# Performance work log

Measured on AMD Instinct MI355X. Metric: run time of the kernel, lower is better.

## Reference

```python
import jax, jax.numpy as jnp
import numpy as np
from jax import lax

B = 2; CIN = 1; IMG = 96; P = 8; EMB = 384; NH = 8; HD = EMB // NH
NL = 6; MLP = 4 * EMB; NC = 2
NPATCH = (IMG // P) ** 3  # 1728
N = NPATCH + 1            # 1729 tokens (cls + patches)


def setup_inputs() -> dict:
    key = jax.random.key(0)
    ks = iter(jax.random.split(key, 16))
    def nrm(shape, scale=0.02):
        return jax.random.normal(next(ks), shape, jnp.float32) * scale
    inp = {}
    inp["x"] = jax.random.normal(next(ks), (B, CIN, IMG, IMG, IMG), jnp.float32)
    inp["conv_w"] = nrm((EMB, CIN, P, P, P))
    inp["conv_b"] = jnp.zeros((EMB,), jnp.float32)
    inp["cls_token"] = nrm((1, 1, EMB))
    inp["pos_embed"] = nrm((1, N, EMB))
    inp["ln1_w"] = jnp.ones((NL, EMB), jnp.float32)
    inp["ln1_b"] = jnp.zeros((NL, EMB), jnp.float32)
    inp["qkv_w"] = nrm((NL, 3 * EMB, EMB))
    inp["qkv_b"] = jnp.zeros((NL, 3 * EMB), jnp.float32)
    inp["proj_w"] = nrm((NL, EMB, EMB))
    inp["proj_b"] = jnp.zeros((NL, EMB), jnp.float32)
    inp["ln2_w"] = jnp.ones((NL, EMB), jnp.float32)
    inp["ln2_b"] = jnp.zeros((NL, EMB), jnp.float32)
    inp["mlp_w1"] = nrm((NL, MLP, EMB))
    inp["mlp_b1"] = jnp.zeros((NL, MLP), jnp.float32)
    inp["mlp_w2"] = nrm((NL, EMB, MLP))
    inp["mlp_b2"] = jnp.zeros((NL, EMB), jnp.float32)
    inp["norm_w"] = jnp.ones((EMB,), jnp.float32)
    inp["norm_b"] = jnp.zeros((EMB,), jnp.float32)
    inp["head_w"] = nrm((NC, EMB))
    inp["head_b"] = jnp.zeros((NC,), jnp.float32)
    return inp


def _ln(x, w, b, eps=1e-5):
    mu = jnp.mean(x, axis=-1, keepdims=True)
    var = jnp.mean((x - mu) ** 2, axis=-1, keepdims=True)
    return (x - mu) * lax.rsqrt(var + eps) * w + b


def reference(x, conv_w, conv_b, cls_token, pos_embed,
              ln1_w, ln1_b, qkv_w, qkv_b, proj_w, proj_b,
              ln2_w, ln2_b, mlp_w1, mlp_b1, mlp_w2, mlp_b2,
              norm_w, norm_b, head_w, head_b):
    b = x.shape[0]
    # Conv3d patch embedding (kernel == stride)
    xp = lax.conv_general_dilated(
        x, conv_w, window_strides=(P, P, P), padding='VALID',
        dimension_numbers=('NCDHW', 'OIDHW', 'NCDHW'))
    xp = xp + conv_b[None, :, None, None, None]
    t = xp.reshape(b, EMB, NPATCH).transpose(0, 2, 1)  # [B, NPATCH, EMB]
    cls = jnp.broadcast_to(cls_token, (b, 1, EMB))
    t = jnp.concatenate([cls, t], axis=1) + pos_embed   # [B, N, EMB]
    scale = HD ** -0.5
    for i in range(NL):
        # --- attention block ---
        h = _ln(t, ln1_w[i], ln1_b[i])
        qkv = (h @ qkv_w[i].T + qkv_b[i]).reshape(b, N, 3, NH, HD)
        q, k, v = qkv[:, :, 0], qkv[:, :, 1], qkv[:, :, 2]  # [B, N, NH, HD]
        scores = jnp.einsum('bnhd,bmhd->bhnm', q, k) * scale
        attn = jax.nn.softmax(scores, axis=-1)
        o = jnp.einsum('bhnm,bmhd->bnhd', attn, v).reshape(b, N, EMB)
        t = t + (o @ proj_w[i].T + proj_b[i])
        # --- MLP block ---
        h = _ln(t, ln2_w[i], ln2_b[i])
        h = jax.nn.gelu(h @ mlp_w1[i].T + mlp_b1[i], approximate=False)
        t = t + (h @ mlp_w2[i].T + mlp_b2[i])
    t = _ln(t, norm_w, norm_b)
    logits = t[:, 0] @ head_w.T + head_b  # [B, NC]
    return logits
```

## Files before the change

kernel.cpp:

```cpp
#include <hip/hip_runtime.h>
#include <math.h>

#define B_      2
#define EMB_    384
#define NH_     8
#define HD_     48
#define NTOK    1729
#define NPATCH_ 1728
#define MLP_    1536
#define NL_     6
#define NC_     2
#define BSTR    1792
#define M_PAD   3584
#define SCALE_  0.14433756729740643f
#define OPSZ    ((size_t)B_ * BSTR * EMB_)

typedef __bf16 bf16x8 __attribute__((ext_vector_type(8)));
typedef float floatx4 __attribute__((ext_vector_type(4)));
typedef _Float16 halfx4 __attribute__((ext_vector_type(4)));
typedef unsigned short u16;

__device__ __forceinline__ u16 f2b(float f) {
    unsigned int u = __float_as_uint(f);
    return (u16)((u + 0x7FFFu + ((u >> 16) & 1u)) >> 16);
}
__device__ __forceinline__ u16 f2h(float f) {
    _Float16 h = (_Float16)f;
    return __builtin_bit_cast(unsigned short, h);
}
__device__ __forceinline__ bf16x8 ld8(const u16* p) {
    return *(const bf16x8*)p;
}

#define CW_N  196608
#define P0_   196608
#define P1_   1966080
#define P2_   4620288
#define P3_   5505024
#define P4_   9043968
#define P5_   12582912
__global__ __launch_bounds__(256) void cvt_all(
    const float* __restrict__ cw, const float* __restrict__ x,
    const float* __restrict__ qw, const float* __restrict__ pw,
    const float* __restrict__ w1, const float* __restrict__ w2,
    u16* __restrict__ cwb, u16* __restrict__ xb, u16* __restrict__ qwb,
    u16* __restrict__ pwb, u16* __restrict__ w1b, u16* __restrict__ w2b)
{
    int i = (blockIdx.x * 256 + threadIdx.x) * 4;
    const float* s; u16* d; int off;
    if      (i < P0_) { s = cw; d = cwb; off = 0; }
    else if (i < P1_) { s = x;  d = xb;  off = P0_; }
    else if (i < P2_) { s = qw; d = qwb; off = P1_; }
    else if (i < P3_) { s = pw; d = pwb; off = P2_; }
    else if (i < P4_) { s = w1; d = w1b; off = P3_; }
    else              { s = w2; d = w2b; off = P4_; }
    i -= off;
    float4 v = *(const float4*)(s + i);
    ushort4 o;
    o.x = f2b(v.x); o.y = f2b(v.y); o.z = f2b(v.z); o.w = f2b(v.w);
    *(ushort4*)(d + i) = o;
}

__global__ __launch_bounds__(256) void patch_mfma(
    const u16* __restrict__ xb, const u16* __restrict__ cwb,
    const float* __restrict__ cb, const float* __restrict__ cls,
    const float* __restrict__ pos, float* __restrict__ t)
{
    __shared__ __align__(16) u16 As[64][40];
    __shared__ __align__(16) u16 Bs[64][40];
    const int tid  = threadIdx.x;
    const int lane = tid & 63, w = tid >> 6;
    const int wm = (w >> 1) * 32, wn = (w & 1) * 32;
    const int m0g = blockIdx.y * 64, n0g = blockIdx.x * 64;
    const int cl = lane & 15, kh = (lane >> 4) * 8;

    if (blockIdx.x == 0 && blockIdx.y == 0) {
        for (int c = tid; c < 2 * EMB_; c += 256) {
            int bb = c / EMB_, e = c % EMB_;
            t[(size_t)bb * BSTR * EMB_ + e] = cls[e] + pos[e];
        }
    }

    const int sm = tid >> 2, skc = tid & 3;
    const int gm_s = m0g + sm;
    const int bb_s = gm_s / 1728, p_s = gm_s % 1728;
    const int pz = p_s / 144, py = (p_s / 12) % 12, px = p_s % 12;

    floatx4 acc[2][2];
#pragma unroll
    for (int i = 0; i < 2; ++i)
#pragma unroll
        for (int j = 0; j < 2; ++j) acc[i][j] = (floatx4){0.f, 0.f, 0.f, 0.f};

    for (int k0 = 0; k0 < 512; k0 += 32) {
        {
            int k = k0 + skc * 8;
            int dz = k >> 6, dy = (k >> 3) & 7;
            *(uint4*)&As[sm][skc * 8] =
                *(const uint4*)(xb + ((size_t)(bb_s * 96 + pz * 8 + dz) * 96 +
                                      py * 8 + dy) * 96 + px * 8);
            *(uint4*)&Bs[sm][skc * 8] =
                *(const uint4*)(cwb + (size_t)(n0g + sm) * 512 + k);
        }
        __syncthreads();
        bf16x8 af[2], bfr[2];
#pragma unroll
        for (int i = 0; i < 2; ++i) af[i] = ld8(&As[wm + 16 * i + cl][kh]);
#pragma unroll
        for (int j = 0; j < 2; ++j) bfr[j] = ld8(&Bs[wn + 16 * j + cl][kh]);
#pragma unroll
        for (int i = 0; i < 2; ++i)
#pragma unroll
            for (int j = 0; j < 2; ++j)
                acc[i][j] = __builtin_amdgcn_mfma_f32_16x16x32_bf16(
                    af[i], bfr[j], acc[i][j], 0, 0, 0);
        __syncthreads();
    }

    const int r0 = (lane >> 4) * 4;
#pragma unroll
    for (int j = 0; j < 2; ++j) {
        int gn = n0g + wn + 16 * j + cl;
        float bn = cb[gn];
#pragma unroll
        for (int i = 0; i < 2; ++i) {
#pragma unroll
            for (int r = 0; r < 4; ++r) {
                int gm = m0g + wm + 16 * i + r0 + r;
                int bb = gm / 1728, p = gm % 1728;
                t[((size_t)bb * BSTR + 1 + p) * EMB_ + gn] =
                    acc[i][j][r] + bn + pos[(size_t)(1 + p) * EMB_ + gn];
            }
        }
    }
}

__global__ __launch_bounds__(256) void ln_kernel(
    const float* __restrict__ x, const float* __restrict__ w,
    const float* __restrict__ b, u16* __restrict__ y)
{
    const int wave = threadIdx.x >> 6;
    const int lane = threadIdx.x & 63;
    const int tok  = blockIdx.x * 4 + wave;
    if (tok >= NTOK) return;
    const size_t row = (size_t)blockIdx.y * BSTR + tok;
    const float* xr = x + row * EMB_;

    float v[6];
    float s = 0.f;
#pragma unroll
    for (int j = 0; j < 6; ++j) { v[j] = xr[lane + 64 * j]; s += v[j]; }
#pragma unroll
    for (int off = 32; off; off >>= 1) s += __shfl_xor(s, off, 64);
    const float mean = s * (1.0f / EMB_);

    float q = 0.f;
#pragma unroll
    for (int j = 0; j < 6; ++j) { float d = v[j] - mean; q += d * d; }
#pragma unroll
    for (int off = 32; off; off >>= 1) q += __shfl_xor(q, off, 64);
    const float rstd = rsqrtf(q * (1.0f / EMB_) + 1e-5f);

    u16* yr = y + row * EMB_;
#pragma unroll
    for (int j = 0; j < 6; ++j) {
        int e = lane + 64 * j;
        yr[e] = f2b((v[j] - mean) * rstd * w[e] + b[e]);
    }
}

template<int FI, int FJ, int ACT, int VT, int RES>
__global__ __launch_bounds__(256) void gemm2(
    const u16* __restrict__ A, const u16* __restrict__ W,
    const float* __restrict__ bias, float* __restrict__ T,
    u16* __restrict__ Cb, u16* __restrict__ vt, int N, int K)
{
    constexpr int TM = 32 * FI;
    constexpr int TN = 32 * FJ;
    __shared__ __align__(16) u16 As[TM][72];
    __shared__ __align__(16) u16 Bs[TN][72];
    const int tid  = threadIdx.x;
    const int lane = tid & 63, w = tid >> 6;
    const int wm = (w >> 1) * (16 * FI);
    const int wn = (w & 1) * (16 * FJ);
    const int m0g = blockIdx.y * TM, n0g = blockIdx.x * TN;
    const int cl = lane & 15, kh = (lane >> 4) * 8;

    floatx4 acc[FI][FJ];
#pragma unroll
    for (int i = 0; i < FI; ++i)
#pragma unroll
        for (int j = 0; j < FJ; ++j)
            acc[i][j] = (floatx4){0.f, 0.f, 0.f, 0.f};

    for (int k0 = 0; k0 < K; k0 += 64) {
#pragma unroll
        for (int u = 0; u < TM / 32; ++u) {
            int c = tid + u * 256;
            int m = c >> 3, kc = c & 7;
            *(uint4*)&As[m][kc * 8] =
                *(const uint4*)(A + (size_t)(m0g + m) * K + k0 + kc * 8);
        }
#pragma unroll
        for (int u = 0; u < TN / 32; ++u) {
            int c = tid + u * 256;
            int n = c >> 3, kc = c & 7;
            *(uint4*)&Bs[n][kc * 8] =
                *(const uint4*)(W + (size_t)(n0g + n) * K + k0 + kc * 8);
        }
        __syncthreads();

        bf16x8 af[FI][2], bfr[FJ][2];
#pragma unroll
        for (int i = 0; i < FI; ++i) {
            af[i][0] = ld8(&As[wm + 16 * i + cl][kh]);
            af[i][1] = ld8(&As[wm + 16 * i + cl][32 + kh]);
        }
#pragma unroll
        for (int j = 0; j < FJ; ++j) {
            bfr[j][0] = ld8(&Bs[wn + 16 * j + cl][kh]);
            bfr[j][1] = ld8(&Bs[wn + 16 * j + cl][32 + kh]);
        }
#pragma unroll
        for (int i = 0; i < FI; ++i)
#pragma unroll
            for (int j = 0; j < FJ; ++j) {
                acc[i][j] = __builtin_amdgcn_mfma_f32_16x16x32_bf16(
                    af[i][0], bfr[j][0], acc[i][j], 0, 0, 0);
                acc[i][j] = __builtin_amdgcn_mfma_f32_16x16x32_bf16(
                    af[i][1], bfr[j][1], acc[i][j], 0, 0, 0);
            }
        __syncthreads();
    }

    const int r0 = (lane >> 4) * 4;
#pragma unroll
    for (int j = 0; j < FJ; ++j) {
        int gn = n0g + wn + 16 * j + cl;
        float bn = bias[gn];
#pragma unroll
        for (int i = 0; i < FI; ++i) {
            int gm0 = m0g + wm + 16 * i + r0;
            if (RES) {
#pragma unroll
                for (int r = 0; r < 4; ++r) {
                    size_t idx = (size_t)(gm0 + r) * EMB_ + gn;
                    T[idx] += acc[i][j][r] + bn;
                }
            } else {
                float v[4];
#pragma unroll
                for (int r = 0; r < 4; ++r) {
                    float vv = acc[i][j][r] + bn;
                    if (ACT) vv = 0.5f * vv * (1.0f + erff(vv * 0.70710678118654752f));
                    v[r] = vv;
                }
                if (VT && gn >= 768) {
                    int hh = (gn - 768) / 48, dd = (gn - 768) % 48;
                    int bb = gm0 / BSTR, tok = gm0 - bb * BSTR;
                    ushort4 o;
                    o.x = f2h(v[0]); o.y = f2h(v[1]);
                    o.z = f2h(v[2]); o.w = f2h(v[3]);
                    *(ushort4*)(vt + ((size_t)(bb * 8 + hh) * 48 + dd) * BSTR + tok) = o;
                } else {
#pragma unroll
                    for (int r = 0; r < 4; ++r)
                        Cb[(size_t)(gm0 + r) * N + gn] = f2b(v[r]);
                }
            }
        }
    }
}

__global__ __launch_bounds__(256) void attn_mfma(
    const u16* __restrict__ big, const u16* __restrict__ vT,
    u16* __restrict__ op, float* __restrict__ lp)
{
    __shared__ __align__(16) u16 qs[64][72];
    __shared__ __align__(16) u16 ks[2][64][72];
    __shared__ __align__(16) u16 vts[2][48][68];

    const int tid  = threadIdx.x;
    const int lane = tid & 63, wave = tid >> 6;
    const int t = lane & 15, quad = lane >> 4;
    const int q0 = blockIdx.x * 64, h = blockIdx.y;
    const int b = blockIdx.z >> 1, sp = blockIdx.z & 1;
    const int tile0 = sp * 14;
    const u16* rowb = big + (size_t)b * BSTR * 1152;
    const u16* vTb  = vT + ((size_t)(b * 8 + h) * 48) * BSTR;

    {
        uint4 z = make_uint4(0, 0, 0, 0);
        for (int c = tid; c < 384; c += 256) {
            int reg = c >> 7, idx = c & 127;
            int rr = idx >> 1, hb = idx & 1;
            if (reg == 0) *(uint4*)&qs[rr][48 + hb * 8] = z;
            else          *(uint4*)&ks[reg - 1][rr][48 + hb * 8] = z;
        }
    }
    for (int c = tid; c < 384; c += 256) {
        int tok = c / 6, ch = c % 6;
        int n = q0 + tok;
        uint4 v = make_uint4(0, 0, 0, 0);
        if (n < NTOK)
            v = *(const uint4*)(rowb + (size_t)n * 1152 + h * 48 + ch * 8);
        *(uint4*)&qs[tok][ch * 8] = v;
    }

    const int c1v = tid + 256;
    const int ktok0 = tid / 6, kch0 = tid % 6;
    const int ktok1 = c1v / 6, kch1 = c1v % 6;
    const int vd0 = tid >> 3,  vch0 = tid & 7;
    const int vd1 = (c1v) >> 3, vch1 = c1v & 7;
    const bool two = (tid < 128);
    uint4 kr0, kr1, vr0, vr1;

#define PREFETCH(K0)                                                          \
    {                                                                         \
        int n0 = (K0) + ktok0;                                                \
        kr0 = (n0 < NTOK) ? *(const uint4*)(rowb + (size_t)n0 * 1152 + 384 +  \
                                            h * 48 + kch0 * 8)                \
                          : make_uint4(0, 0, 0, 0);                           \
        vr0 = *(const uint4*)(vTb + (size_t)vd0 * BSTR + (K0) + vch0 * 8);    \
        if (two) {                                                            \
            int n1 = (K0) + ktok1;                                            \
            kr1 = (n1 < NTOK) ? *(const uint4*)(rowb + (size_t)n1 * 1152 +    \
                                                384 + h * 48 + kch1 * 8)      \
                              : make_uint4(0, 0, 0, 0);                       \
            vr1 = *(const uint4*)(vTb + (size_t)vd1 * BSTR + (K0) + vch1 * 8);\
        }                                                                     \
    }
#define COMMIT(BUF)                                                           \
    {                                                                         \
        *(uint4*)&ks[BUF][ktok0][kch0 * 8] = kr0;                             \
        *(uint4*)&vts[BUF][vd0][vch0 * 8] = vr0;                              \
        if (two) {                                                            \
            *(uint4*)&ks[BUF][ktok1][kch1 * 8] = kr1;                         \
            *(uint4*)&vts[BUF][vd1][vch1 * 8] = vr1;                          \
        }                                                                     \
    }

    PREFETCH(tile0 * 64);
    COMMIT(0);
    __syncthreads();

    float l_lane = 0.f;
    floatx4 oacc[3];
#pragma unroll
    for (int dt = 0; dt < 3; ++dt) oacc[dt] = (floatx4){0.f, 0.f, 0.f, 0.f};

    for (int it = 0; it < 14; ++it) {
        const int k0 = (tile0 + it) * 64;
        const int cur = it & 1, nxt = cur ^ 1;
        if (it < 13) PREFETCH(k0 + 64);

        floatx4 sf[4];
#pragma unroll
        for (int f = 0; f < 4; ++f) sf[f] = (floatx4){0.f, 0.f, 0.f, 0.f};
        bf16x8 qb0 = ld8(&qs[wave * 16 + t][quad * 8]);
        bf16x8 qb1 = ld8(&qs[wave * 16 + t][32 + quad * 8]);
#pragma unroll
        for (int f = 0; f < 4; ++f) {
            bf16x8 ka0 = ld8(&ks[cur][f * 16 + t][quad * 8]);
            bf16x8 ka1 = ld8(&ks[cur][f * 16 + t][32 + quad * 8]);
            sf[f] = __builtin_amdgcn_mfma_f32_16x16x32_bf16(ka0, qb0, sf[f], 0, 0, 0);
            sf[f] = __builtin_amdgcn_mfma_f32_16x16x32_bf16(ka1, qb1, sf[f], 0, 0, 0);
        }
        if (k0 + 64 > NTOK) {
#pragma unroll
            for (int f = 0; f < 4; ++f)
#pragma unroll
                for (int r = 0; r < 4; ++r) {
                    bool valid = (k0 + f * 16 + quad * 4 + r) < NTOK;
                    if (!valid) sf[f][r] = -1e30f;
                }
        }
#pragma unroll
        for (int f = 0; f < 4; ++f)
#pragma unroll
            for (int r = 0; r < 4; ++r) {
                sf[f][r] = __expf(sf[f][r] * SCALE_);
                l_lane += sf[f][r];
            }

#pragma unroll
        for (int f = 0; f < 4; ++f) {
            halfx4 pa;
            pa[0] = (_Float16)sf[f][0]; pa[1] = (_Float16)sf[f][1];
            pa[2] = (_Float16)sf[f][2]; pa[3] = (_Float16)sf[f][3];
#pragma unroll
            for (int dt = 0; dt < 3; ++dt) {
                ushort4 vv = *(const ushort4*)&vts[cur][dt * 16 + t][f * 16 + quad * 4];
                halfx4 vb = __builtin_bit_cast(halfx4, vv);
                oacc[dt] = __builtin_amdgcn_mfma_f32_16x16x16f16(pa, vb, oacc[dt], 0, 0, 0);
            }
        }

        if (it < 13) COMMIT(nxt);
        __syncthreads();
    }
#undef PREFETCH
#undef COMMIT

    l_lane += __shfl_xor(l_lane, 16, 64);
    l_lane += __shfl_xor(l_lane, 32, 64);
    if (quad == 0)
        lp[((size_t)(sp * B_ + b) * BSTR + q0 + wave * 16 + t) * NH_ + h] = l_lane;

#pragma unroll
    for (int r = 0; r < 4; ++r) {
        int n = q0 + wave * 16 + quad * 4 + r;
        if (n >= NTOK) continue;
#pragma unroll
        for (int dt = 0; dt < 3; ++dt)
            op[((size_t)(sp * B_ + b) * BSTR + n) * EMB_ + h * 48 + dt * 16 + t] =
                f2h(oacc[dt][r]);
    }
}

__global__ __launch_bounds__(256) void attn_combine(
    const u16* __restrict__ op, const float* __restrict__ lp,
    u16* __restrict__ ao)
{
    int g = blockIdx.x * 256 + threadIdx.x;
    int e4 = g % 96;
    int rem = g / 96;
    int n = rem % BSTR;
    int b = rem / BSTR;
    int e = e4 * 4;
    size_t base = ((size_t)b * BSTR + n) * EMB_ + e;
    if (n >= NTOK) {
        *(ushort4*)(ao + base) = make_ushort4(0, 0, 0, 0);
        return;
    }
    int h = e / 48;
    ushort4 a4 = *(const ushort4*)(op + base);
    ushort4 b4 = *(const ushort4*)(op + OPSZ + base);
    halfx4 ha = __builtin_bit_cast(halfx4, a4);
    halfx4 hb = __builtin_bit_cast(halfx4, b4);
    float l0 = lp[((size_t)b * BSTR + n) * NH_ + h];
    float l1 = lp[((size_t)(B_ + b) * BSTR + n) * NH_ + h];
    float rinv = 1.0f / (l0 + l1);
    ushort4 o;
    o.x = f2b(((float)ha[0] + (float)hb[0]) * rinv);
    o.y = f2b(((float)ha[1] + (float)hb[1]) * rinv);
    o.z = f2b(((float)ha[2] + (float)hb[2]) * rinv);
    o.w = f2b(((float)ha[3] + (float)hb[3]) * rinv);
    *(ushort4*)(ao + base) = o;
}

__global__ __launch_bounds__(384) void head_kernel(
    const float* __restrict__ t, const float* __restrict__ nw,
    const float* __restrict__ nb, const float* __restrict__ hw,
    const float* __restrict__ hb, float* __restrict__ out)
{
    const int b = blockIdx.x;
    const int e = threadIdx.x;
    const int wave = e >> 6, lane = e & 63;
    __shared__ float red[6];
    __shared__ float nbuf[EMB_];

    float v = t[(size_t)b * BSTR * EMB_ + e];

    float s = v;
#pragma unroll
    for (int off = 32; off; off >>= 1) s += __shfl_xor(s, off, 64);
    if (lane == 0) red[wave] = s;
    __syncthreads();
    float tot = 0.f;
    for (int w2 = 0; w2 < 6; ++w2) tot += red[w2];
    const float mean = tot * (1.0f / EMB_);
    __syncthreads();

    float d = v - mean;
    float q = d * d;
#pragma unroll
    for (int off = 32; off; off >>= 1) q += __shfl_xor(q, off, 64);
    if (lane == 0) red[wave] = q;
    __syncthreads();
    float qt = 0.f;
    for (int w2 = 0; w2 < 6; ++w2) qt += red[w2];
    const float rstd = rsqrtf(qt * (1.0f / EMB_) + 1e-5f);
    nbuf[e] = d * rstd * nw[e] + nb[e];
    __syncthreads();

    for (int c = 0; c < NC_; ++c) {
        float p = nbuf[e] * hw[c * EMB_ + e];
#pragma unroll
        for (int off = 32; off; off >>= 1) p += __shfl_xor(p, off, 64);
        __syncthreads();
        if (lane == 0) red[wave] = p;
        __syncthreads();
        if (e == 0) {
            float sum = 0.f;
            for (int w2 = 0; w2 < 6; ++w2) sum += red[w2];
            out[b * NC_ + c] = sum + hb[c];
        }
    }
}

extern "C" void kernel_launch(void* const* d_in, const int* in_sizes, int n_in,
                              void* d_out, int out_size, void* d_ws, size_t ws_size,
                              hipStream_t stream)
{
    const float* x         = (const float*)d_in[0];
    const float* conv_w    = (const float*)d_in[1];
    const float* conv_b    = (const float*)d_in[2];
    const float* cls_token = (const float*)d_in[3];
    const float* pos_embed = (const float*)d_in[4];
    const float* ln1_w     = (const float*)d_in[5];
    const float* ln1_b     = (const float*)d_in[6];
    const float* qkv_w     = (const float*)d_in[7];
    const float* qkv_b     = (const float*)d_in[8];
    const float* proj_w    = (const float*)d_in[9];
    const float* proj_b    = (const float*)d_in[10];
    const float* ln2_w     = (const float*)d_in[11];
    const float* ln2_b     = (const float*)d_in[12];
    const float* mlp_w1    = (const float*)d_in[13];
    const float* mlp_b1    = (const float*)d_in[14];
    const float* mlp_w2    = (const float*)d_in[15];
    const float* mlp_b2    = (const float*)d_in[16];
    const float* norm_w    = (const float*)d_in[17];
    const float* norm_b    = (const float*)d_in[18];
    const float* head_w    = (const float*)d_in[19];
    const float* head_b    = (const float*)d_in[20];
    float* out = (float*)d_out;

    char* p = (char*)d_ws;
    float* t  = (float*)p;  p += (size_t)M_PAD * EMB_ * 4;
    u16* h    = (u16*)p;    p += (size_t)M_PAD * EMB_ * 2;
    u16* big  = (u16*)p;    p += (size_t)M_PAD * MLP_ * 2;
    u16* ao   = (u16*)p;    p += (size_t)M_PAD * EMB_ * 2;
    u16* wqb  = (u16*)p;    p += (size_t)NL_ * 1152 * EMB_ * 2;
    u16* wpb  = (u16*)p;    p += (size_t)NL_ * EMB_ * EMB_ * 2;
    u16* w1b  = (u16*)p;    p += (size_t)NL_ * MLP_ * EMB_ * 2;
    u16* w2b  = (u16*)p;    p += (size_t)NL_ * EMB_ * MLP_ * 2;
    u16* cwb  = (u16*)p;    p += (size_t)CW_N * 2;
    u16* xb   = (u16*)p;    p += (size_t)B_ * 96 * 96 * 96 * 2;
    u16* op   = (u16*)p;    p += 2 * OPSZ * 2;
    float* lp = (float*)p;  p += (size_t)2 * B_ * BSTR * NH_ * 4;
    u16* vT = big + (size_t)M_PAD * 1152;

    cvt_all<<<P5_ / 4 / 256, 256, 0, stream>>>(
        conv_w, x, qkv_w, proj_w, mlp_w1, mlp_w2,
        cwb, xb, wqb, wpb, w1b, w2b);

    patch_mfma<<<dim3(EMB_ / 64, 3456 / 64), 256, 0, stream>>>(
        xb, cwb, conv_b, cls_token, pos_embed, t);

    const dim3 ln_grid((NTOK + 3) / 4, B_);
    for (int l = 0; l < NL_; ++l) {
        ln_kernel<<<ln_grid, 256, 0, stream>>>(t, ln1_w + l * EMB_, ln1_b + l * EMB_, h);
        gemm2<2, 4, 0, 1, 0><<<dim3(1152 / 128, M_PAD / 64), 256, 0, stream>>>(
            h, wqb + (size_t)l * 1152 * EMB_, qkv_b + l * 1152,
            nullptr, big, vT, 1152, EMB_);
        attn_mfma<<<dim3(BSTR / 64, NH_, B_ * 2), 256, 0, stream>>>(big, vT, op, lp);
        attn_combine<<<(int)(OPSZ / 4 / 256), 256, 0, stream>>>(op, lp, ao);
        gemm2<1, 2, 0, 0, 1><<<dim3(EMB_ / 64, M_PAD / 32), 256, 0, stream>>>(
            ao, wpb + (size_t)l * EMB_ * EMB_, proj_b + l * EMB_,
            t, nullptr, nullptr, EMB_, EMB_);
        ln_kernel<<<ln_grid, 256, 0, stream>>>(t, ln2_w + l * EMB_, ln2_b + l * EMB_, h);
        gemm2<2, 4, 1, 0, 0><<<dim3(MLP_ / 128, M_PAD / 64), 256, 0, stream>>>(
            h, w1b + (size_t)l * MLP_ * EMB_, mlp_b1 + l * MLP_,
            nullptr, big, nullptr, MLP_, EMB_);
        gemm2<1, 2, 0, 0, 1><<<dim3(EMB_ / 64, M_PAD / 32), 256, 0, stream>>>(
            big, w2b + (size_t)l * EMB_ * MLP_, mlp_b2 + l * EMB_,
            t, nullptr, nullptr, EMB_, MLP_);
    }

    head_kernel<<<B_, 384, 0, stream>>>(t, norm_w, norm_b, head_w, head_b, out);
}
```

Before: 659.9 us.

## Fuse attention combine and LayerNorm into full-row residual GEMMs

Adds a gemm_row kernel in which one block computes a full 384-column output row tile, so the residual add can be followed by LayerNorm in the epilogue and the next normalized activations written directly. The proj GEMM also folds in the split-softmax combine while loading its A operand, which removes the attn_combine kernel, the separate ln_kernel launches, and the ao buffer. It also switches the softmax to exp2f with a prescaled constant. In exchange, blocks now cover 32 full rows (112 blocks), which lowers parallelism, and the LayerNorm uses a single-pass E[x²]−mean² variance.

```diff
diff --git a/kernel.cpp b/kernel.cpp
--- a/kernel.cpp
+++ b/kernel.cpp
@@ -12,7 +12,7 @@
 #define NC_     2
 #define BSTR    1792
 #define M_PAD   3584
-#define SCALE_  0.14433756729740643f
+#define SCALE2_ 0.20823661461464808f
 #define OPSZ    ((size_t)B_ * BSTR * EMB_)
 
 typedef __bf16 bf16x8 __attribute__((ext_vector_type(8)));
@@ -23,6 +23,9 @@
 __device__ __forceinline__ u16 f2b(float f) {
     unsigned int u = __float_as_uint(f);
     return (u16)((u + 0x7FFFu + ((u >> 16) & 1u)) >> 16);
+}
+__device__ __forceinline__ float b2f(u16 u) {
+    return __uint_as_float(((unsigned int)u) << 16);
 }
 __device__ __forceinline__ u16 f2h(float f) {
     _Float16 h = (_Float16)f;
@@ -169,11 +172,11 @@
     }
 }
 
-template<int FI, int FJ, int ACT, int VT, int RES>
+template<int FI, int FJ, int ACT, int VT>
 __global__ __launch_bounds__(256) void gemm2(
     const u16* __restrict__ A, const u16* __restrict__ W,
-    const float* __restrict__ bias, float* __restrict__ T,
-    u16* __restrict__ Cb, u16* __restrict__ vt, int N, int K)
+    const float* __restrict__ bias, u16* __restrict__ Cb,
+    u16* __restrict__ vt, int N, int K)
 {
     constexpr int TM = 32 * FI;
     constexpr int TN = 32 * FJ;
@@ -241,33 +244,153 @@
 #pragma unroll
         for (int i = 0; i < FI; ++i) {
             int gm0 = m0g + wm + 16 * i + r0;
-            if (RES) {
-#pragma unroll
-                for (int r = 0; r < 4; ++r) {
-                    size_t idx = (size_t)(gm0 + r) * EMB_ + gn;
-                    T[idx] += acc[i][j][r] + bn;
-                }
+            float v[4];
+#pragma unroll
+            for (int r = 0; r < 4; ++r) {
+                float vv = acc[i][j][r] + bn;
+                if (ACT) vv = 0.5f * vv * (1.0f + erff(vv * 0.70710678118654752f));
+                v[r] = vv;
+            }
+            if (VT && gn >= 768) {
+                int hh = (gn - 768) / 48, dd = (gn - 768) % 48;
+                int bb = gm0 / BSTR, tok = gm0 - bb * BSTR;
+                ushort4 o;
+                o.x = f2h(v[0]); o.y = f2h(v[1]);
+                o.z = f2h(v[2]); o.w = f2h(v[3]);
+                *(ushort4*)(vt + ((size_t)(bb * 8 + hh) * 48 + dd) * BSTR + tok) = o;
             } else {
-                float v[4];
-#pragma unroll
-                for (int r = 0; r < 4; ++r) {
-                    float vv = acc[i][j][r] + bn;
-                    if (ACT) vv = 0.5f * vv * (1.0f + erff(vv * 0.70710678118654752f));
-                    v[r] = vv;
-                }
-                if (VT && gn >= 768) {
-                    int hh = (gn - 768) / 48, dd = (gn - 768) % 48;
-                    int bb = gm0 / BSTR, tok = gm0 - bb * BSTR;
-                    ushort4 o;
-                    o.x = f2h(v[0]); o.y = f2h(v[1]);
-                    o.z = f2h(v[2]); o.w = f2h(v[3]);
-                    *(ushort4*)(vt + ((size_t)(bb * 8 + hh) * 48 + dd) * BSTR + tok) = o;
-                } else {
-#pragma unroll
-                    for (int r = 0; r < 4; ++r)
-                        Cb[(size_t)(gm0 + r) * N + gn] = f2b(v[r]);
-                }
+#pragma unroll
+                for (int r = 0; r < 4; ++r)
+                    Cb[(size_t)(gm0 + r) * N + gn] = f2b(v[r]);
             }
+        }
+    }
+}
+
+template<int COMB, int KK>
+__global__ __launch_bounds__(256) void gemm_row(
+    const u16* __restrict__ A, const u16* __restrict__ op,
+    const float* __restrict__ lp, const u16* __restrict__ W,
+    const float* __restrict__ bias, float* __restrict__ T,
+    const float* __restrict__ lnw, const float* __restrict__ lnb,
+    u16* __restrict__ h)
+{
+    __shared__ __align__(16) u16 As[32][72];
+    __shared__ __align__(16) u16 Bs[384][72];
+    __shared__ float redS[2][32], redQ[2][32];
+    const int tid  = threadIdx.x;
+    const int lane = tid & 63, w = tid >> 6;
+    const int wm = (w >> 1) * 16;
+    const int wn = (w & 1) * 192;
+    const int m0g = blockIdx.x * 32;
+    const int cl = lane & 15, quad = lane >> 4, kh = quad * 8;
+
+    floatx4 acc[12];
+#pragma unroll
+    for (int j = 0; j < 12; ++j) acc[j] = (floatx4){0.f, 0.f, 0.f, 0.f};
+
+    const int am = tid >> 3, akc = tid & 7;
+    const int arow = m0g + am;
+
+    for (int k0 = 0; k0 < KK; k0 += 64) {
+        {
+            int kg = k0 + akc * 8;
+            if (COMB) {
+                int hh = kg / 48;
+                const u16* o0 = op + (size_t)arow * EMB_ + kg;
+                ushort4 x0 = *(const ushort4*)o0;
+                ushort4 x1 = *(const ushort4*)(o0 + 4);
+                ushort4 y0 = *(const ushort4*)(o0 + OPSZ);
+                ushort4 y1 = *(const ushort4*)(o0 + OPSZ + 4);
+                halfx4 a0 = __builtin_bit_cast(halfx4, x0);
+                halfx4 a1 = __builtin_bit_cast(halfx4, x1);
+                halfx4 b0 = __builtin_bit_cast(halfx4, y0);
+                halfx4 b1 = __builtin_bit_cast(halfx4, y1);
+                float l0 = lp[(size_t)arow * NH_ + hh];
+                float l1 = lp[((size_t)M_PAD + arow) * NH_ + hh];
+                float rinv = 1.0f / (l0 + l1);
+                ushort4 lo, hi;
+                lo.x = f2b(((float)a0[0] + (float)b0[0]) * rinv);
+                lo.y = f2b(((float)a0[1] + (float)b0[1]) * rinv);
+                lo.z = f2b(((float)a0[2] + (float)b0[2]) * rinv);
+                lo.w = f2b(((float)a0[3] + (float)b0[3]) * rinv);
+                hi.x = f2b(((float)a1[0] + (float)b1[0]) * rinv);
+                hi.y = f2b(((float)a1[1] + (float)b1[1]) * rinv);
+                hi.z = f2b(((float)a1[2] + (float)b1[2]) * rinv);
+                hi.w = f2b(((float)a1[3] + (float)b1[3]) * rinv);
+                *(ushort4*)&As[am][akc * 8]     = lo;
+                *(ushort4*)&As[am][akc * 8 + 4] = hi;
+            } else {
+                *(uint4*)&As[am][akc * 8] =
+                    *(const uint4*)(A + (size_t)arow * KK + kg);
+            }
+        }
+#pragma unroll
+        for (int u = 0; u < 12; ++u) {
+            int c = tid + u * 256;
+            int n = c >> 3, kc = c & 7;
+            *(uint4*)&Bs[n][kc * 8] =
+                *(const uint4*)(W + (size_t)n * KK + k0 + kc * 8);
+        }
+        __syncthreads();
+
+        bf16x8 af0 = ld8(&As[wm + cl][kh]);
+        bf16x8 af1 = ld8(&As[wm + cl][32 + kh]);
+#pragma unroll
+        for (int j = 0; j < 12; ++j) {
+            bf16x8 b0 = ld8(&Bs[wn + 16 * j + cl][kh]);
+            bf16x8 b1 = ld8(&Bs[wn + 16 * j + cl][32 + kh]);
+            acc[j] = __builtin_amdgcn_mfma_f32_16x16x32_bf16(af0, b0, acc[j], 0, 0, 0);
+            acc[j] = __builtin_amdgcn_mfma_f32_16x16x32_bf16(af1, b1, acc[j], 0, 0, 0);
+        }
+        __syncthreads();
+    }
+
+    const int r0 = quad * 4;
+    float v[12][4];
+    float rs[4] = {0.f, 0.f, 0.f, 0.f}, rq[4] = {0.f, 0.f, 0.f, 0.f};
+#pragma unroll
+    for (int j = 0; j < 12; ++j) {
+        int gn = wn + 16 * j + cl;
+        float bn = bias[gn];
+#pragma unroll
+        for (int r = 0; r < 4; ++r) {
+            size_t idx = (size_t)(m0g + wm + r0 + r) * EMB_ + gn;
+            float vv = acc[j][r] + bn + T[idx];
+            T[idx] = vv;
+            v[j][r] = vv;
+            rs[r] += vv;
+            rq[r] += vv * vv;
+        }
+    }
+#pragma unroll
+    for (int off = 1; off < 16; off <<= 1)
+#pragma unroll
+        for (int r = 0; r < 4; ++r) {
+            rs[r] += __shfl_xor(rs[r], off, 64);
+            rq[r] += __shfl_xor(rq[r], off, 64);
+        }
+    if (cl == 0) {
+#pragma unroll
+        for (int r = 0; r < 4; ++r) {
+            redS[w & 1][wm + r0 + r] = rs[r];
+            redQ[w & 1][wm + r0 + r] = rq[r];
+        }
+    }
+    __syncthreads();
+#pragma unroll
+    for (int r = 0; r < 4; ++r) {
+        int lr = wm + r0 + r;
+        float s = redS[0][lr] + redS[1][lr];
+        float q = redQ[0][lr] + redQ[1][lr];
+        float mu = s * (1.0f / EMB_);
+        float va = fmaxf(q * (1.0f / EMB_) - mu * mu, 0.f);
+        float rstd = rsqrtf(va + 1e-5f);
+        u16* hr = h + (size_t)(m0g + lr) * EMB_;
+#pragma unroll
+        for (int j = 0; j < 12; ++j) {
+            int gn = wn + 16 * j + cl;
+            hr[gn] = f2b((v[j][r] - mu) * rstd * lnw[gn] + lnb[gn]);
         }
     }
 }
@@ -379,7 +502,7 @@
         for (int f = 0; f < 4; ++f)
 #pragma unroll
             for (int r = 0; r < 4; ++r) {
-                sf[f][r] = __expf(sf[f][r] * SCALE_);
+                sf[f][r] = exp2f(sf[f][r] * SCALE2_);
                 l_lane += sf[f][r];
             }
 
@@ -410,7 +533,6 @@
 #pragma unroll
     for (int r = 0; r < 4; ++r) {
         int n = q0 + wave * 16 + quad * 4 + r;
-        if (n >= NTOK) continue;
 #pragma unroll
         for (int dt = 0; dt < 3; ++dt)
             op[((size_t)(sp * B_ + b) * BSTR + n) * EMB_ + h * 48 + dt * 16 + t] =
@@ -418,74 +540,19 @@
     }
 }
 
-__global__ __launch_bounds__(256) void attn_combine(
-    const u16* __restrict__ op, const float* __restrict__ lp,
-    u16* __restrict__ ao)
-{
-    int g = blockIdx.x * 256 + threadIdx.x;
-    int e4 = g % 96;
-    int rem = g / 96;
-    int n = rem % BSTR;
-    int b = rem / BSTR;
-    int e = e4 * 4;
-    size_t base = ((size_t)b * BSTR + n) * EMB_ + e;
-    if (n >= NTOK) {
-        *(ushort4*)(ao + base) = make_ushort4(0, 0, 0, 0);
-        return;
-    }
-    int h = e / 48;
-    ushort4 a4 = *(const ushort4*)(op + base);
-    ushort4 b4 = *(const ushort4*)(op + OPSZ + base);
-    halfx4 ha = __builtin_bit_cast(halfx4, a4);
-    halfx4 hb = __builtin_bit_cast(halfx4, b4);
-    float l0 = lp[((size_t)b * BSTR + n) * NH_ + h];
-    float l1 = lp[((size_t)(B_ + b) * BSTR + n) * NH_ + h];
-    float rinv = 1.0f / (l0 + l1);
-    ushort4 o;
-    o.x = f2b(((float)ha[0] + (float)hb[0]) * rinv);
-    o.y = f2b(((float)ha[1] + (float)hb[1]) * rinv);
-    o.z = f2b(((float)ha[2] + (float)hb[2]) * rinv);
-    o.w = f2b(((float)ha[3] + (float)hb[3]) * rinv);
-    *(ushort4*)(ao + base) = o;
-}
-
 __global__ __launch_bounds__(384) void head_kernel(
-    const float* __restrict__ t, const float* __restrict__ nw,
-    const float* __restrict__ nb, const float* __restrict__ hw,
+    const u16* __restrict__ h, const float* __restrict__ hw,
     const float* __restrict__ hb, float* __restrict__ out)
 {
     const int b = blockIdx.x;
     const int e = threadIdx.x;
     const int wave = e >> 6, lane = e & 63;
     __shared__ float red[6];
-    __shared__ float nbuf[EMB_];
-
-    float v = t[(size_t)b * BSTR * EMB_ + e];
-
-    float s = v;
-#pragma unroll
-    for (int off = 32; off; off >>= 1) s += __shfl_xor(s, off, 64);
-    if (lane == 0) red[wave] = s;
-    __syncthreads();
-    float tot = 0.f;
-    for (int w2 = 0; w2 < 6; ++w2) tot += red[w2];
-    const float mean = tot * (1.0f / EMB_);
-    __syncthreads();
-
-    float d = v - mean;
-    float q = d * d;
-#pragma unroll
-    for (int off = 32; off; off >>= 1) q += __shfl_xor(q, off, 64);
-    if (lane == 0) red[wave] = q;
-    __syncthreads();
-    float qt = 0.f;
-    for (int w2 = 0; w2 < 6; ++w2) qt += red[w2];
-    const float rstd = rsqrtf(qt * (1.0f / EMB_) + 1e-5f);
-    nbuf[e] = d * rstd * nw[e] + nb[e];
-    __syncthreads();
+
+    float v = b2f(h[(size_t)b * BSTR * EMB_ + e]);
 
     for (int c = 0; c < NC_; ++c) {
-        float p = nbuf[e] * hw[c * EMB_ + e];
+        float p = v * hw[c * EMB_ + e];
 #pragma unroll
         for (int off = 32; off; off >>= 1) p += __shfl_xor(p, off, 64);
         __syncthreads();
@@ -530,7 +597,6 @@
     float* t  = (float*)p;  p += (size_t)M_PAD * EMB_ * 4;
     u16* h    = (u16*)p;    p += (size_t)M_PAD * EMB_ * 2;
     u16* big  = (u16*)p;    p += (size_t)M_PAD * MLP_ * 2;
-    u16* ao   = (u16*)p;    p += (size_t)M_PAD * EMB_ * 2;
     u16* wqb  = (u16*)p;    p += (size_t)NL_ * 1152 * EMB_ * 2;
     u16* wpb  = (u16*)p;    p += (size_t)NL_ * EMB_ * EMB_ * 2;
     u16* w1b  = (u16*)p;    p += (size_t)NL_ * MLP_ * EMB_ * 2;
@@ -548,25 +614,25 @@
     patch_mfma<<<dim3(EMB_ / 64, 3456 / 64), 256, 0, stream>>>(
         xb, cwb, conv_b, cls_token, pos_embed, t);
 
-    const dim3 ln_grid((NTOK + 3) / 4, B_);
+    ln_kernel<<<dim3((NTOK + 3) / 4, B_), 256, 0, stream>>>(
+        t, ln1_w, ln1_b, h);
+
     for (int l = 0; l < NL_; ++l) {
-        ln_kernel<<<ln_grid, 256, 0, stream>>>(t, ln1_w + l * EMB_, ln1_b + l * EMB_, h);
-        gemm2<2, 4, 0, 1, 0><<<dim3(1152 / 128, M_PAD / 64), 256, 0, stream>>>(
-            h, wqb + (size_t)l * 1152 * EMB_, qkv_b + l * 1152,
-            nullptr, big, vT, 1152, EMB_);
+        gemm2<2, 4, 0, 1><<<dim3(1152 / 128, M_PAD / 64), 256, 0, stream>>>(
+            h, wqb + (size_t)l * 1152 * EMB_, qkv_b + l * 1152, big, vT, 1152, EMB_);
         attn_mfma<<<dim3(BSTR / 64, NH_, B_ * 2), 256, 0, stream>>>(big, vT, op, lp);
-        attn_combine<<<(int)(OPSZ / 4 / 256), 256, 0, stream>>>(op, lp, ao);
-        gemm2<1, 2, 0, 0, 1><<<dim3(EMB_ / 64, M_PAD / 32), 256, 0, stream>>>(
-            ao, wpb + (size_t)l * EMB_ * EMB_, proj_b + l * EMB_,
-            t, nullptr, nullptr, EMB_, EMB_);
-        ln_kernel<<<ln_grid, 256, 0, stream>>>(t, ln2_w + l * EMB_, ln2_b + l * EMB_, h);
-        gemm2<2, 4, 1, 0, 0><<<dim3(MLP_ / 128, M_PAD / 64), 256, 0, stream>>>(
-            h, w1b + (size_t)l * MLP_ * EMB_, mlp_b1 + l * MLP_,
-            nullptr, big, nullptr, MLP_, EMB_);
-        gemm2<1, 2, 0, 0, 1><<<dim3(EMB_ / 64, M_PAD / 32), 256, 0, stream>>>(
-            big, w2b + (size_t)l * EMB_ * MLP_, mlp_b2 + l * EMB_,
-            t, nullptr, nullptr, EMB_, MLP_);
-    }
-
-    head_kernel<<<B_, 384, 0, stream>>>(t, norm_w, norm_b, head_w, head_b, out);
-}
+        gemm_row<1, EMB_><<<M_PAD / 32, 256, 0, stream>>>(
+            big, op, lp, wpb + (size_t)l * EMB_ * EMB_, proj_b + l * EMB_,
+            t, ln2_w + l * EMB_, ln2_b + l * EMB_, h);
+        gemm2<2, 4, 1, 0><<<dim3(MLP_ / 128, M_PAD / 64), 256, 0, stream>>>(
+            h, w1b + (size_t)l * MLP_ * EMB_, mlp_b1 + l * MLP_, big, nullptr,
+            MLP_, EMB_);
+        const float* nlw = (l < NL_ - 1) ? (ln1_w + (l + 1) * EMB_) : norm_w;
+        const float* nlb = (l < NL_ - 1) ? (ln1_b + (l + 1) * EMB_) : norm_b;
+        gemm_row<0, MLP_><<<M_PAD / 32, 256, 0, stream>>>(
+            big, nullptr, nullptr, w2b + (size_t)l * EMB_ * MLP_,
+            mlp_b2 + l * EMB_, t, nlw, nlb, h);
+    }
+
+    head_kernel<<<B_, 384, 0, stream>>>(h, head_w, head_b, out);
+}
```

Result: slower. 805.6 us (+22.1%).

## Double-buffer GEMM tiles, split attention KV four ways, shrink GEMM N tiles

Applied to the files above, without the earlier changes.

The GEMM kernel now stages the next K tile in registers while MFMAs run on the current shared-memory buffer, hiding global-load latency behind compute. Attention splits the key range into four parts instead of two, which raises the number of blocks, and the combine kernel sums four partials. The QKV and MLP1 GEMMs use narrower 64-column tiles to launch more blocks. exp is replaced by exp2 with a pre-scaled constant. The costs are double the shared memory in the GEMM, more partial-output traffic, and a longer combine pass.

```diff
diff --git a/kernel.cpp b/kernel.cpp
--- a/kernel.cpp
+++ b/kernel.cpp
@@ -12,8 +12,9 @@
 #define NC_     2
 #define BSTR    1792
 #define M_PAD   3584
-#define SCALE_  0.14433756729740643f
+#define SCALE2_ 0.20823661461464808f
 #define OPSZ    ((size_t)B_ * BSTR * EMB_)
+#define NSPLIT  4
 
 typedef __bf16 bf16x8 __attribute__((ext_vector_type(8)));
 typedef float floatx4 __attribute__((ext_vector_type(4)));
@@ -177,8 +178,10 @@
 {
     constexpr int TM = 32 * FI;
     constexpr int TN = 32 * FJ;
-    __shared__ __align__(16) u16 As[TM][72];
-    __shared__ __align__(16) u16 Bs[TN][72];
+    constexpr int NA = TM / 32;
+    constexpr int NB = TN / 32;
+    __shared__ __align__(16) u16 As[2][TM][72];
+    __shared__ __align__(16) u16 Bs[2][TN][72];
     const int tid  = threadIdx.x;
     const int lane = tid & 63, w = tid >> 6;
     const int wm = (w >> 1) * (16 * FI);
@@ -186,6 +189,36 @@
     const int m0g = blockIdx.y * TM, n0g = blockIdx.x * TN;
     const int cl = lane & 15, kh = (lane >> 4) * 8;
 
+    uint4 ra[NA], rb[NB];
+    auto pref = [&](int k0) {
+#pragma unroll
+        for (int u = 0; u < NA; ++u) {
+            int c = tid + u * 256;
+            int m = c >> 3, kc = c & 7;
+            ra[u] = *(const uint4*)(A + (size_t)(m0g + m) * K + k0 + kc * 8);
+        }
+#pragma unroll
+        for (int u = 0; u < NB; ++u) {
+            int c = tid + u * 256;
+            int n = c >> 3, kc = c & 7;
+            rb[u] = *(const uint4*)(W + (size_t)(n0g + n) * K + k0 + kc * 8);
+        }
+    };
+    auto commit = [&](int buf) {
+#pragma unroll
+        for (int u = 0; u < NA; ++u) {
+            int c = tid + u * 256;
+            int m = c >> 3, kc = c & 7;
+            *(uint4*)&As[buf][m][kc * 8] = ra[u];
+        }
+#pragma unroll
+        for (int u = 0; u < NB; ++u) {
+            int c = tid + u * 256;
+            int n = c >> 3, kc = c & 7;
+            *(uint4*)&Bs[buf][n][kc * 8] = rb[u];
+        }
+    };
+
     floatx4 acc[FI][FJ];
 #pragma unroll
     for (int i = 0; i < FI; ++i)
@@ -193,33 +226,25 @@
         for (int j = 0; j < FJ; ++j)
             acc[i][j] = (floatx4){0.f, 0.f, 0.f, 0.f};
 
-    for (int k0 = 0; k0 < K; k0 += 64) {
-#pragma unroll
-        for (int u = 0; u < TM / 32; ++u) {
-            int c = tid + u * 256;
-            int m = c >> 3, kc = c & 7;
-            *(uint4*)&As[m][kc * 8] =
-                *(const uint4*)(A + (size_t)(m0g + m) * K + k0 + kc * 8);
-        }
-#pragma unroll
-        for (int u = 0; u < TN / 32; ++u) {
-            int c = tid + u * 256;
-            int n = c >> 3, kc = c & 7;
-            *(uint4*)&Bs[n][kc * 8] =
-                *(const uint4*)(W + (size_t)(n0g + n) * K + k0 + kc * 8);
-        }
-        __syncthreads();
+    pref(0);
+    commit(0);
+    __syncthreads();
+
+    const int NIT = K >> 6;
+    for (int it = 0; it < NIT; ++it) {
+        const int cur = it & 1, nxt = cur ^ 1;
+        if (it + 1 < NIT) pref((it + 1) * 64);
 
         bf16x8 af[FI][2], bfr[FJ][2];
 #pragma unroll
         for (int i = 0; i < FI; ++i) {
-            af[i][0] = ld8(&As[wm + 16 * i + cl][kh]);
-            af[i][1] = ld8(&As[wm + 16 * i + cl][32 + kh]);
+            af[i][0] = ld8(&As[cur][wm + 16 * i + cl][kh]);
+            af[i][1] = ld8(&As[cur][wm + 16 * i + cl][32 + kh]);
         }
 #pragma unroll
         for (int j = 0; j < FJ; ++j) {
-            bfr[j][0] = ld8(&Bs[wn + 16 * j + cl][kh]);
-            bfr[j][1] = ld8(&Bs[wn + 16 * j + cl][32 + kh]);
+            bfr[j][0] = ld8(&Bs[cur][wn + 16 * j + cl][kh]);
+            bfr[j][1] = ld8(&Bs[cur][wn + 16 * j + cl][32 + kh]);
         }
 #pragma unroll
         for (int i = 0; i < FI; ++i)
@@ -230,6 +255,8 @@
                 acc[i][j] = __builtin_amdgcn_mfma_f32_16x16x32_bf16(
                     af[i][1], bfr[j][1], acc[i][j], 0, 0, 0);
             }
+
+        if (it + 1 < NIT) commit(nxt);
         __syncthreads();
     }
 
@@ -284,8 +311,8 @@
     const int lane = tid & 63, wave = tid >> 6;
     const int t = lane & 15, quad = lane >> 4;
     const int q0 = blockIdx.x * 64, h = blockIdx.y;
-    const int b = blockIdx.z >> 1, sp = blockIdx.z & 1;
-    const int tile0 = sp * 14;
+    const int b = blockIdx.z >> 2, sp = blockIdx.z & 3;
+    const int tile0 = sp * 7;
     const u16* rowb = big + (size_t)b * BSTR * 1152;
     const u16* vTb  = vT + ((size_t)(b * 8 + h) * 48) * BSTR;
 
@@ -349,10 +376,10 @@
 #pragma unroll
     for (int dt = 0; dt < 3; ++dt) oacc[dt] = (floatx4){0.f, 0.f, 0.f, 0.f};
 
-    for (int it = 0; it < 14; ++it) {
+    for (int it = 0; it < 7; ++it) {
         const int k0 = (tile0 + it) * 64;
         const int cur = it & 1, nxt = cur ^ 1;
-        if (it < 13) PREFETCH(k0 + 64);
+        if (it < 6) PREFETCH(k0 + 64);
 
         floatx4 sf[4];
 #pragma unroll
@@ -379,7 +406,7 @@
         for (int f = 0; f < 4; ++f)
 #pragma unroll
             for (int r = 0; r < 4; ++r) {
-                sf[f][r] = __expf(sf[f][r] * SCALE_);
+                sf[f][r] = exp2f(sf[f][r] * SCALE2_);
                 l_lane += sf[f][r];
             }
 
@@ -396,7 +423,7 @@
             }
         }
 
-        if (it < 13) COMMIT(nxt);
+        if (it < 6) COMMIT(nxt);
         __syncthreads();
     }
 #undef PREFETCH
@@ -410,7 +437,6 @@
 #pragma unroll
     for (int r = 0; r < 4; ++r) {
         int n = q0 + wave * 16 + quad * 4 + r;
-        if (n >= NTOK) continue;
 #pragma unroll
         for (int dt = 0; dt < 3; ++dt)
             op[((size_t)(sp * B_ + b) * BSTR + n) * EMB_ + h * 48 + dt * 16 + t] =
@@ -434,18 +460,22 @@
         return;
     }
     int h = e / 48;
-    ushort4 a4 = *(const ushort4*)(op + base);
-    ushort4 b4 = *(const ushort4*)(op + OPSZ + base);
-    halfx4 ha = __builtin_bit_cast(halfx4, a4);
-    halfx4 hb = __builtin_bit_cast(halfx4, b4);
-    float l0 = lp[((size_t)b * BSTR + n) * NH_ + h];
-    float l1 = lp[((size_t)(B_ + b) * BSTR + n) * NH_ + h];
-    float rinv = 1.0f / (l0 + l1);
+    float osum[4] = {0.f, 0.f, 0.f, 0.f};
+    float ltot = 0.f;
+#pragma unroll
+    for (int s = 0; s < NSPLIT; ++s) {
+        ushort4 a4 = *(const ushort4*)(op + (size_t)s * OPSZ + base);
+        halfx4 ha = __builtin_bit_cast(halfx4, a4);
+#pragma unroll
+        for (int k = 0; k < 4; ++k) osum[k] += (float)ha[k];
+        ltot += lp[((size_t)(s * B_ + b) * BSTR + n) * NH_ + h];
+    }
+    float rinv = 1.0f / ltot;
     ushort4 o;
-    o.x = f2b(((float)ha[0] + (float)hb[0]) * rinv);
-    o.y = f2b(((float)ha[1] + (float)hb[1]) * rinv);
-    o.z = f2b(((float)ha[2] + (float)hb[2]) * rinv);
-    o.w = f2b(((float)ha[3] + (float)hb[3]) * rinv);
+    o.x = f2b(osum[0] * rinv);
+    o.y = f2b(osum[1] * rinv);
+    o.z = f2b(osum[2] * rinv);
+    o.w = f2b(osum[3] * rinv);
     *(ushort4*)(ao + base) = o;
 }
 
@@ -537,8 +567,8 @@
     u16* w2b  = (u16*)p;    p += (size_t)NL_ * EMB_ * MLP_ * 2;
     u16* cwb  = (u16*)p;    p += (size_t)CW_N * 2;
     u16* xb   = (u16*)p;    p += (size_t)B_ * 96 * 96 * 96 * 2;
-    u16* op   = (u16*)p;    p += 2 * OPSZ * 2;
-    float* lp = (float*)p;  p += (size_t)2 * B_ * BSTR * NH_ * 4;
+    u16* op   = (u16*)p;    p += NSPLIT * OPSZ * 2;
+    float* lp = (float*)p;  p += (size_t)NSPLIT * B_ * BSTR * NH_ * 4;
     u16* vT = big + (size_t)M_PAD * 1152;
 
     cvt_all<<<P5_ / 4 / 256, 256, 0, stream>>>(
@@ -551,16 +581,16 @@
     const dim3 ln_grid((NTOK + 3) / 4, B_);
     for (int l = 0; l < NL_; ++l) {
         ln_kernel<<<ln_grid, 256, 0, stream>>>(t, ln1_w + l * EMB_, ln1_b + l * EMB_, h);
-        gemm2<2, 4, 0, 1, 0><<<dim3(1152 / 128, M_PAD / 64), 256, 0, stream>>>(
+        gemm2<2, 2, 0, 1, 0><<<dim3(1152 / 64, M_PAD / 64), 256, 0, stream>>>(
             h, wqb + (size_t)l * 1152 * EMB_, qkv_b + l * 1152,
             nullptr, big, vT, 1152, EMB_);
-        attn_mfma<<<dim3(BSTR / 64, NH_, B_ * 2), 256, 0, stream>>>(big, vT, op, lp);
+        attn_mfma<<<dim3(BSTR / 64, NH_, B_ * NSPLIT), 256, 0, stream>>>(big, vT, op, lp);
         attn_combine<<<(int)(OPSZ / 4 / 256), 256, 0, stream>>>(op, lp, ao);
         gemm2<1, 2, 0, 0, 1><<<dim3(EMB_ / 64, M_PAD / 32), 256, 0, stream>>>(
             ao, wpb + (size_t)l * EMB_ * EMB_, proj_b + l * EMB_,
             t, nullptr, nullptr, EMB_, EMB_);
         ln_kernel<<<ln_grid, 256, 0, stream>>>(t, ln2_w + l * EMB_, ln2_b + l * EMB_, h);
-        gemm2<2, 4, 1, 0, 0><<<dim3(MLP_ / 128, M_PAD / 64), 256, 0, stream>>>(
+        gemm2<2, 2, 1, 0, 0><<<dim3(MLP_ / 64, M_PAD / 64), 256, 0, stream>>>(
             h, w1b + (size_t)l * MLP_ * EMB_, mlp_b1 + l * MLP_,
             nullptr, big, nullptr, MLP_, EMB_);
         gemm2<1, 2, 0, 0, 1><<<dim3(EMB_ / 64, M_PAD / 32), 256, 0, stream>>>(
```

Result: slower. 1.185 ms (+79.6%).
